# Performance work log

Measured on AMD Instinct MI355X. Metric: run time of the kernel, lower is better.

The kernel has to match this reference:

```python
import jax, jax.numpy as jnp
import numpy as np

L, M, B = 32768, 8, 8192      # lines, max neighbors per line, blocks
LIN, BIN, H = 768, 768, 512   # line_in_dim, block_in_dim, hidden_size
NH, DH = 8, 512 // 8          # heads, head_dim
LN_EPS = 1e-5


def _ln(x, g, b):
    mu = jnp.mean(x, axis=-1, keepdims=True)
    var = jnp.mean(jnp.square(x - mu), axis=-1, keepdims=True)
    return (x - mu) * jax.lax.rsqrt(var + LN_EPS) * g + b


def setup_inputs() -> dict:
    key = jax.random.key(0)
    ks = jax.random.split(key, 12)
    w = lambda k, shape, fan: jax.random.normal(k, shape, jnp.float32) * (fan ** -0.5)
    return {
        'global_lines': jax.random.normal(ks[0], (L, LIN), jnp.float32),
        'block_reprs': jax.random.normal(ks[1], (B, BIN), jnp.float32),
        'Wq': w(ks[2], (H, LIN), LIN),            # q_proj (no bias)
        'Wkv': w(ks[3], (H, BIN), BIN),           # kv_proj (no bias)
        'qn_g': jnp.ones((H,), jnp.float32), 'qn_b': jnp.zeros((H,), jnp.float32),
        'kvn_g': jnp.ones((H,), jnp.float32), 'kvn_b': jnp.zeros((H,), jnp.float32),
        'in_proj_w': w(ks[4], (3 * H, H), H), 'in_proj_b': jnp.zeros((3 * H,), jnp.float32),
        'out_w': w(ks[5], (H, H), H), 'out_b': jnp.zeros((H,), jnp.float32),
        'p1_w': w(ks[6], (H, 2 * H), 2 * H), 'p1_b': jnp.zeros((H,), jnp.float32),
        'ln1_g': jnp.ones((H,), jnp.float32), 'ln1_b': jnp.zeros((H,), jnp.float32),
        'p2_w': w(ks[7], (H, H), H), 'p2_b': jnp.zeros((H,), jnp.float32),
        'ln2_g': jnp.ones((H,), jnp.float32), 'ln2_b': jnp.zeros((H,), jnp.float32),
        'head_w': w(ks[8], (1, H), H), 'head_b': jnp.zeros((1,), jnp.float32),
        'K_indices': jax.random.randint(ks[9], (L, M), 0, B, jnp.int32),
        'neighbor_counts': jnp.clip(jax.random.randint(ks[10], (L,), 0, M + 1, jnp.int32), 1, M),
    }


def reference(global_lines, block_reprs, Wq, Wkv, qn_g, qn_b, kvn_g, kvn_b,
              in_proj_w, in_proj_b, out_w, out_b,
              p1_w, p1_b, ln1_g, ln1_b, p2_w, p2_b, ln2_g, ln2_b,
              head_w, head_b, K_indices, neighbor_counts):
    # q = LN(q_proj(lines))                              [L, H]
    q = _ln(global_lines @ Wq.T, qn_g, qn_b)
    # gather neighbor block reprs, project, LN           [L, M, H]
    kv = _ln(block_reprs[K_indices] @ Wkv.T, kvn_g, kvn_b)
    pad = jnp.arange(M)[None, :] >= neighbor_counts[:, None]  # True = padded key

    # torch nn.MultiheadAttention with query length 1 per line
    wq_i, wk_i, wv_i = jnp.split(in_proj_w, 3, axis=0)
    bq_i, bk_i, bv_i = jnp.split(in_proj_b, 3, axis=0)
    qh = (q @ wq_i.T + bq_i).reshape(L, NH, DH)
    kh = (kv @ wk_i.T + bk_i).reshape(L, M, NH, DH)
    vh = (kv @ wv_i.T + bv_i).reshape(L, M, NH, DH)
    scores = jnp.einsum('lhd,lmhd->lhm', qh, kh) / np.float32(np.sqrt(DH))
    scores = jnp.where(pad[:, None, :], jnp.finfo(scores.dtype).min, scores)
    attn = jax.nn.softmax(scores, axis=-1)
    ctx = jnp.einsum('lhm,lmhd->lhd', attn, vh).reshape(L, H)
    attn_out = ctx @ out_w.T + out_b

    # line_proj: Linear(2H->H) + LN + GELU + residual(Linear + LN + GELU)
    x = jnp.concatenate([q, attn_out], axis=-1)
    x = jax.nn.gelu(_ln(x @ p1_w.T + p1_b, ln1_g, ln1_b), approximate=False)
    x = x + jax.nn.gelu(_ln(x @ p2_w.T + p2_b, ln2_g, ln2_b), approximate=False)
    logits = (x @ head_w.T + head_b)[:, 0]
    return jax.nn.sigmoid(logits)
```

## Files before the change

### kernel.cpp

```cpp
#include <hip/hip_runtime.h>
#include <math.h>


typedef unsigned short u16;
typedef unsigned int u32;
using bf16x8 = __attribute__((ext_vector_type(8))) __bf16;
using u16x8  = __attribute__((ext_vector_type(8))) u16;
using f32x4  = __attribute__((ext_vector_type(4))) float;

__device__ __forceinline__ u16 f2bf(float f) {
    u32 u = __builtin_bit_cast(u32, f);
    u32 r = u + 0x7fffu + ((u >> 16) & 1u);
    return (u16)(r >> 16);
}
__device__ __forceinline__ float bf2f(u16 h) {
    return __builtin_bit_cast(float, (u32)h << 16);
}
__device__ __forceinline__ float gelu_exact(float x) {
    return 0.5f * x * (1.0f + erff(x * 0.70710678118654752440f));
}

__device__ __forceinline__ float breduce1(float s0, float* sm) {
    #pragma unroll
    for (int off = 32; off > 0; off >>= 1) s0 += __shfl_down(s0, off);
    const int lane = threadIdx.x & 63, w = threadIdx.x >> 6;
    __syncthreads();
    if (lane == 0) sm[w] = s0;
    __syncthreads();
    return sm[0] + sm[1] + sm[2] + sm[3];
}

struct CvtJobs {
    const float* s[5];
    u16* d[5];
    int cum[6];
};
__global__ __launch_bounds__(256) void cvt_multi(CvtJobs j)
{
    const int g = blockIdx.x * 256 + threadIdx.x;
    if (g >= j.cum[5]) return;
    int seg = 0;
    #pragma unroll
    for (int k = 1; k < 5; ++k) seg += (g >= j.cum[k]);
    const int q = g - j.cum[seg];
    const float4 v = *reinterpret_cast<const float4*>(j.s[seg] + q * 4);
    ushort4 o = make_ushort4(f2bf(v.x), f2bf(v.y), f2bf(v.z), f2bf(v.w));
    *reinterpret_cast<ushort4*>(j.d[seg] + q * 4) = o;
}

__global__ __launch_bounds__(256) void fold_w2(
    const float* __restrict__ p1w, const float* __restrict__ outw,
    u16* __restrict__ p1cb)
{
    __shared__ float As[16][65];
    __shared__ float Bs[16][65];
    const int tx = threadIdx.x & 15, ty = threadIdx.x >> 4;
    const int i0 = blockIdx.y * 64, j0 = blockIdx.x * 64;
    const int lr = threadIdx.x >> 2;
    const int lc = (threadIdx.x & 3) * 4;
    const int kr = threadIdx.x >> 4;
    const int jc = (threadIdx.x & 15) * 4;
    float acc[4][4] = {};
    for (int k0 = 0; k0 < 512; k0 += 16) {
        const float4 av = *reinterpret_cast<const float4*>(
            p1w + (size_t)(i0 + lr) * 1024 + 512 + k0 + lc);
        As[lc + 0][lr] = av.x; As[lc + 1][lr] = av.y;
        As[lc + 2][lr] = av.z; As[lc + 3][lr] = av.w;
        const float4 bv = *reinterpret_cast<const float4*>(
            outw + (size_t)(k0 + kr) * 512 + j0 + jc);
        Bs[kr][jc + 0] = bv.x; Bs[kr][jc + 1] = bv.y;
        Bs[kr][jc + 2] = bv.z; Bs[kr][jc + 3] = bv.w;
        __syncthreads();
        #pragma unroll
        for (int kk = 0; kk < 16; ++kk) {
            float a[4], b[4];
            #pragma unroll
            for (int i = 0; i < 4; ++i) a[i] = As[kk][ty * 4 + i];
            #pragma unroll
            for (int jj = 0; jj < 4; ++jj) b[jj] = Bs[kk][tx * 4 + jj];
            #pragma unroll
            for (int i = 0; i < 4; ++i)
                #pragma unroll
                for (int jj = 0; jj < 4; ++jj)
                    acc[i][jj] = fmaf(a[i], b[jj], acc[i][jj]);
        }
        __syncthreads();
    }
    #pragma unroll
    for (int i = 0; i < 4; ++i)
        #pragma unroll
        for (int jj = 0; jj < 4; ++jj)
            p1cb[(size_t)(i0 + ty * 4 + i) * 1024 + 512 + j0 + tx * 4 + jj] =
                f2bf(acc[i][jj]);
}

__global__ __launch_bounds__(64) void fold_bias(
    const float* __restrict__ p1w, const float* __restrict__ outb,
    const float* __restrict__ p1b, float* __restrict__ bias2)
{
    const int i = blockIdx.x, lane = threadIdx.x;
    float s = 0.0f;
    #pragma unroll
    for (int k = lane; k < 512; k += 64)
        s += p1w[(size_t)i * 1024 + 512 + k] * outb[k];
    #pragma unroll
    for (int off = 32; off > 0; off >>= 1) s += __shfl_down(s, off);
    if (lane == 0) bias2[i] = s + p1b[i];
}

template<int A_MODE, bool STATS>
__global__ __launch_bounds__(256) void gemm_bf16(
    const void* __restrict__ A1v, const void* __restrict__ A2v, int K1, int K,
    const u16* __restrict__ W, const float* __restrict__ bias,
    u16* __restrict__ C, int N, float* __restrict__ stats)
{
    __shared__ __bf16 As[128 * 32];
    __shared__ __bf16 Ws[128 * 32];
    const int tid = threadIdx.x;
    const int w = tid >> 6, lane = tid & 63;

    const u32 nx = gridDim.x;
    const u32 orig = blockIdx.y * nx + blockIdx.x;
    const u32 nwg = nx * gridDim.y;
    const u32 wgid = (orig & 7u) * (nwg >> 3) + (orig >> 3);
    const int bx = wgid % nx;
    const int row0 = (int)(wgid / nx) * 128;
    const int col0 = bx * 128;

    const int wr = (w >> 1) * 64, wc = (w & 1) * 64;
    const int fr = lane & 15, fg = lane >> 4;

    int srow[2], scol[2], soff[2];
    #pragma unroll
    for (int c = 0; c < 2; ++c) {
        const int bo = w * 2048 + c * 1024 + lane * 16;
        srow[c] = bo >> 6;
        scol[c] = (bo & 63) >> 1;
        soff[c] = (w * 2048 + c * 1024) >> 1;
    }
    const int ar = tid >> 1;
    const int ac = (tid & 1) * 16;

    f32x4 acc[4][4] = {};

    for (int k0 = 0; k0 < K; k0 += 32) {
        if (A_MODE == 1) {
            const float* Af = (const float*)A1v;
            const float* src = Af + (size_t)(row0 + ar) * K + k0 + ac;
            const float4 v0 = *reinterpret_cast<const float4*>(src);
            const float4 v1 = *reinterpret_cast<const float4*>(src + 4);
            const float4 v2 = *reinterpret_cast<const float4*>(src + 8);
            const float4 v3 = *reinterpret_cast<const float4*>(src + 12);
            u16x8 p0, p1;
            p0[0] = f2bf(v0.x); p0[1] = f2bf(v0.y); p0[2] = f2bf(v0.z); p0[3] = f2bf(v0.w);
            p0[4] = f2bf(v1.x); p0[5] = f2bf(v1.y); p0[6] = f2bf(v1.z); p0[7] = f2bf(v1.w);
            p1[0] = f2bf(v2.x); p1[1] = f2bf(v2.y); p1[2] = f2bf(v2.z); p1[3] = f2bf(v2.w);
            p1[4] = f2bf(v3.x); p1[5] = f2bf(v3.y); p1[6] = f2bf(v3.z); p1[7] = f2bf(v3.w);
            *reinterpret_cast<u16x8*>((u16*)As + ar * 32 + ac) = p0;
            *reinterpret_cast<u16x8*>((u16*)As + ar * 32 + ac + 8) = p1;
        } else {
            #pragma unroll
            for (int c = 0; c < 2; ++c) {
                const u16* asrc;
                if (A_MODE == 2) {
                    const bool first = (k0 < K1);
                    const u16* base = first ? (const u16*)A1v : (const u16*)A2v;
                    const int ldk = first ? K1 : (K - K1);
                    const int kk  = first ? k0 : (k0 - K1);
                    asrc = base + (size_t)(row0 + srow[c]) * ldk + kk + scol[c];
                } else {
                    asrc = (const u16*)A1v + (size_t)(row0 + srow[c]) * K + k0 + scol[c];
                }
                __builtin_amdgcn_global_load_lds(
                    (const __attribute__((address_space(1))) u32*)asrc,
                    (__attribute__((address_space(3))) u32*)(As + soff[c]), 16, 0, 0);
            }
        }
        #pragma unroll
        for (int c = 0; c < 2; ++c) {
            const u16* wsrc = W + (size_t)(col0 + srow[c]) * K + k0 + scol[c];
            __builtin_amdgcn_global_load_lds(
                (const __attribute__((address_space(1))) u32*)wsrc,
                (__attribute__((address_space(3))) u32*)(Ws + soff[c]), 16, 0, 0);
        }
        __syncthreads();

        bf16x8 af[4], bfr[4];
        #pragma unroll
        for (int m = 0; m < 4; ++m) {
            af[m]  = *(const bf16x8*)(As + (wr + m * 16 + fr) * 32 + fg * 8);
            bfr[m] = *(const bf16x8*)(Ws + (wc + m * 16 + fr) * 32 + fg * 8);
        }
        #pragma unroll
        for (int m = 0; m < 4; ++m)
            #pragma unroll
            for (int n = 0; n < 4; ++n)
                acc[m][n] = __builtin_amdgcn_mfma_f32_16x16x32_bf16(
                    af[m], bfr[n], acc[m][n], 0, 0, 0);
        __syncthreads();
    }

    if (bias) {
        #pragma unroll
        for (int n = 0; n < 4; ++n) {
            const float bv = bias[col0 + wc + n * 16 + fr];
            #pragma unroll
            for (int m = 0; m < 4; ++m)
                #pragma unroll
                for (int r = 0; r < 4; ++r)
                    acc[m][n][r] += bv;
        }
    }

    #pragma unroll
    for (int m = 0; m < 4; ++m)
        #pragma unroll
        for (int n = 0; n < 4; ++n) {
            const int col = col0 + wc + n * 16 + fr;
            #pragma unroll
            for (int r = 0; r < 4; ++r) {
                const int row = row0 + wr + m * 16 + fg * 4 + r;
                C[(size_t)row * N + col] = f2bf(acc[m][n][r]);
            }
        }

    if (STATS) {
        float ps[4][4], pq[4][4];
        #pragma unroll
        for (int m = 0; m < 4; ++m)
            #pragma unroll
            for (int r = 0; r < 4; ++r) {
                float s = 0.0f, q2 = 0.0f;
                #pragma unroll
                for (int n = 0; n < 4; ++n) {
                    const float v = acc[m][n][r];
                    s += v; q2 = fmaf(v, v, q2);
                }
                ps[m][r] = s; pq[m][r] = q2;
            }
        #pragma unroll
        for (int off = 1; off < 16; off <<= 1)
            #pragma unroll
            for (int m = 0; m < 4; ++m)
                #pragma unroll
                for (int r = 0; r < 4; ++r) {
                    ps[m][r] += __shfl_xor(ps[m][r], off);
                    pq[m][r] += __shfl_xor(pq[m][r], off);
                }
        if (fr == 0) {
            const int cb = bx * 2 + (w & 1);
            #pragma unroll
            for (int m = 0; m < 4; ++m)
                #pragma unroll
                for (int r = 0; r < 4; ++r) {
                    const int row = row0 + wr + m * 16 + fg * 4 + r;
                    *reinterpret_cast<float2*>(stats + ((size_t)row * 8 + cb) * 2) =
                        make_float2(ps[m][r], pq[m][r]);
                }
        }
    }
}

template<bool GELU>
__global__ __launch_bounds__(256) void ln_rows_s(
    u16* __restrict__ X, const float* __restrict__ stats,
    const float* __restrict__ g, const float* __restrict__ b)
{
    const size_t row = blockIdx.x;
    float s = 0.0f, q2 = 0.0f;
    #pragma unroll
    for (int cb = 0; cb < 8; ++cb) {
        s  += stats[(row * 8 + cb) * 2];
        q2 += stats[(row * 8 + cb) * 2 + 1];
    }
    const float mu = s * (1.0f / 512.0f);
    const float var = q2 * (1.0f / 512.0f) - mu * mu;
    const float rs = rsqrtf(var + 1e-5f);
    const int t = threadIdx.x;
    const ushort2 xv = *reinterpret_cast<const ushort2*>(X + row * 512 + 2 * t);
    const float2 gg = *reinterpret_cast<const float2*>(g + 2 * t);
    const float2 bb = *reinterpret_cast<const float2*>(b + 2 * t);
    float y0 = (bf2f(xv.x) - mu) * rs * gg.x + bb.x;
    float y1 = (bf2f(xv.y) - mu) * rs * gg.y + bb.y;
    if (GELU) { y0 = gelu_exact(y0); y1 = gelu_exact(y1); }
    *reinterpret_cast<ushort2*>(X + row * 512 + 2 * t) = make_ushort2(f2bf(y0), f2bf(y1));
}

__global__ __launch_bounds__(512) void attn_kernel(
    const u16* __restrict__ qh, const u16* __restrict__ kvb,
    const int* __restrict__ kidx, const int* __restrict__ ncnt,
    u16* __restrict__ ctx)
{
    const int head = threadIdx.x >> 6;
    const int lane = threadIdx.x & 63;
    const int mi = lane & 7, dg = lane >> 3;
    const bool b0 = (mi & 1), b1 = (mi & 2), b2 = (mi & 4);
    const int doff = (b0 ? 4 : 0) + (b1 ? 2 : 0) + (b2 ? 1 : 0);

    for (int l = blockIdx.x; l < 32768; l += gridDim.x) {
        const int cnt = ncnt[l];
        const int idx = kidx[l * 8 + mi];
        const size_t kvbase = (size_t)idx * 1024 + head * 64 + dg * 8;

        const u16x8 qv = *(const u16x8*)(qh + (size_t)l * 512 + head * 64 + dg * 8);
        const u16x8 kv = *(const u16x8*)(kvb + kvbase);
        const u16x8 vv = *(const u16x8*)(kvb + kvbase + 512);

        float p = 0.0f;
        #pragma unroll
        for (int jj = 0; jj < 8; ++jj) p = fmaf(bf2f(qv[jj]), bf2f(kv[jj]), p);
        p += __shfl_xor(p, 8); p += __shfl_xor(p, 16); p += __shfl_xor(p, 32);

        float s = (mi < cnt) ? p * 0.125f : -3.402823466e38f;
        float mx = s;
        mx = fmaxf(mx, __shfl_xor(mx, 1));
        mx = fmaxf(mx, __shfl_xor(mx, 2));
        mx = fmaxf(mx, __shfl_xor(mx, 4));
        const float e = __expf(s - mx);
        float den = e;
        den += __shfl_xor(den, 1); den += __shfl_xor(den, 2); den += __shfl_xor(den, 4);
        const float wgt = e / den;

        float c[8];
        #pragma unroll
        for (int jj = 0; jj < 8; ++jj) c[jj] = wgt * bf2f(vv[jj]);

        #pragma unroll
        for (int jj = 0; jj < 4; ++jj) {
            const float snd = b0 ? c[jj] : c[jj + 4];
            const float rec = __shfl_xor(snd, 1);
            c[jj] = (b0 ? c[jj + 4] : c[jj]) + rec;
        }
        #pragma unroll
        for (int jj = 0; jj < 2; ++jj) {
            const float snd = b1 ? c[jj] : c[jj + 2];
            const float rec = __shfl_xor(snd, 2);
            c[jj] = (b1 ? c[jj + 2] : c[jj]) + rec;
        }
        {
            const float snd = b2 ? c[0] : c[1];
            const float rec = __shfl_xor(snd, 4);
            c[0] = (b2 ? c[1] : c[0]) + rec;
        }
        ctx[(size_t)l * 512 + head * 64 + dg * 8 + doff] = f2bf(c[0]);
    }
}

__global__ __launch_bounds__(256) void final_head_s(
    const u16* __restrict__ h1, const u16* __restrict__ h2raw,
    const float* __restrict__ stats,
    const float* __restrict__ g, const float* __restrict__ b,
    const float* __restrict__ hw, const float* __restrict__ hb,
    float* __restrict__ out)
{
    __shared__ float sm[4];
    const size_t row = blockIdx.x;
    float s = 0.0f, q2 = 0.0f;
    #pragma unroll
    for (int cb = 0; cb < 8; ++cb) {
        s  += stats[(row * 8 + cb) * 2];
        q2 += stats[(row * 8 + cb) * 2 + 1];
    }
    const float mu = s * (1.0f / 512.0f);
    const float var = q2 * (1.0f / 512.0f) - mu * mu;
    const float rs = rsqrtf(var + 1e-5f);
    const int t = threadIdx.x;
    const ushort2 xv = *reinterpret_cast<const ushort2*>(h2raw + row * 512 + 2 * t);
    const ushort2 hv = *reinterpret_cast<const ushort2*>(h1 + row * 512 + 2 * t);
    const float2 gg = *reinterpret_cast<const float2*>(g + 2 * t);
    const float2 bb = *reinterpret_cast<const float2*>(b + 2 * t);
    const float2 hwv = *reinterpret_cast<const float2*>(hw + 2 * t);
    const float y0 = bf2f(hv.x) + gelu_exact((bf2f(xv.x) - mu) * rs * gg.x + bb.x);
    const float y1 = bf2f(hv.y) + gelu_exact((bf2f(xv.y) - mu) * rs * gg.y + bb.y);
    const float d = breduce1(y0 * hwv.x + y1 * hwv.y, sm);
    if (t == 0) out[row] = 1.0f / (1.0f + expf(-(d + hb[0])));
}

extern "C" void kernel_launch(void* const* d_in, const int* in_sizes, int n_in,
                              void* d_out, int out_size, void* d_ws, size_t ws_size,
                              hipStream_t stream)
{
    const float* lines  = (const float*)d_in[0];
    const float* blocks = (const float*)d_in[1];
    const float* Wq     = (const float*)d_in[2];
    const float* Wkv    = (const float*)d_in[3];
    const float* qn_g   = (const float*)d_in[4];
    const float* qn_b   = (const float*)d_in[5];
    const float* kvn_g  = (const float*)d_in[6];
    const float* kvn_b  = (const float*)d_in[7];
    const float* in_w   = (const float*)d_in[8];
    const float* in_b   = (const float*)d_in[9];
    const float* out_w  = (const float*)d_in[10];
    const float* out_b  = (const float*)d_in[11];
    const float* p1_w   = (const float*)d_in[12];
    const float* p1_b   = (const float*)d_in[13];
    const float* ln1_g  = (const float*)d_in[14];
    const float* ln1_b  = (const float*)d_in[15];
    const float* p2_w   = (const float*)d_in[16];
    const float* p2_b   = (const float*)d_in[17];
    const float* ln2_g  = (const float*)d_in[18];
    const float* ln2_b  = (const float*)d_in[19];
    const float* head_w = (const float*)d_in[20];
    const float* head_b = (const float*)d_in[21];
    const int*   kidx   = (const int*)d_in[22];
    const int*   ncnt   = (const int*)d_in[23];
    float* out = (float*)d_out;

    char* wsb = (char*)d_ws;
    u16* qb    = (u16*)(wsb);
    u16* qhb   = (u16*)(wsb + (32ull << 20));
    u16* ctxb  = (u16*)(wsb + (64ull << 20));
    u16* kvbb  = (u16*)(wsb + (96ull << 20));
    u16* bkvb  = (u16*)(wsb + (112ull << 20));
    float* stats_q   = (float*)(wsb + (120ull << 20));
    float* stats_h1  = (float*)(wsb + (124ull << 20));
    float* stats_h2  = (float*)(wsb + (128ull << 20));
    float* stats_bkv = (float*)(wsb + (132ull << 20));
    u16* Wqb   = (u16*)(wsb + (136ull << 20));
    u16* Wkvb  = Wqb + 512 * 768;
    u16* inwb  = Wkvb + 512 * 768;
    u16* p1cb  = inwb + 1536 * 512;
    u16* p2wb  = p1cb + 512 * 1024;
    float* bias2f = (float*)(p2wb + 512 * 512);

    {
        CvtJobs j;
        const float* ss[5] = { Wq, Wkv, in_w, p1_w, p2_w };
        u16* dd[5] = { Wqb, Wkvb, inwb, p1cb, p2wb };
        const int nn[5] = { 512 * 768, 512 * 768, 1536 * 512, 512 * 1024, 512 * 512 };
        int c = 0;
        for (int k = 0; k < 5; ++k) { j.s[k] = ss[k]; j.d[k] = dd[k]; j.cum[k] = c; c += nn[k] / 4; }
        j.cum[5] = c;
        cvt_multi<<<(c + 255) / 256, 256, 0, stream>>>(j);
    }
    fold_w2<<<dim3(8, 8), 256, 0, stream>>>(p1_w, out_w, p1cb);
    fold_bias<<<512, 64, 0, stream>>>(p1_w, out_b, p1_b, bias2f);

    gemm_bf16<1, true><<<dim3(4, 64), 256, 0, stream>>>(
        blocks, nullptr, 768, 768, Wkvb, nullptr, bkvb, 512, stats_bkv);
    ln_rows_s<false><<<8192, 256, 0, stream>>>(bkvb, stats_bkv, kvn_g, kvn_b);
    gemm_bf16<0, false><<<dim3(8, 64), 256, 0, stream>>>(
        bkvb, nullptr, 512, 512, inwb + 512 * 512, in_b + 512, kvbb, 1024, nullptr);
    gemm_bf16<1, true><<<dim3(4, 256), 256, 0, stream>>>(
        lines, nullptr, 768, 768, Wqb, nullptr, qb, 512, stats_q);
    ln_rows_s<false><<<32768, 256, 0, stream>>>(qb, stats_q, qn_g, qn_b);
    gemm_bf16<0, false><<<dim3(4, 256), 256, 0, stream>>>(
        qb, nullptr, 512, 512, inwb, in_b, qhb, 512, nullptr);
    attn_kernel<<<2048, 512, 0, stream>>>(qhb, kvbb, kidx, ncnt, ctxb);
    gemm_bf16<2, true><<<dim3(4, 256), 256, 0, stream>>>(
        qb, ctxb, 512, 1024, p1cb, bias2f, qhb, 512, stats_h1);
    ln_rows_s<true><<<32768, 256, 0, stream>>>(qhb, stats_h1, ln1_g, ln1_b);
    gemm_bf16<0, true><<<dim3(4, 256), 256, 0, stream>>>(
        qhb, nullptr, 512, 512, p2wb, p2_b, ctxb, 512, stats_h2);
    final_head_s<<<32768, 256, 0, stream>>>(qhb, ctxb, stats_h2, ln2_g, ln2_b,
                                            head_w, head_b, out);
}
```

Before: 467.2 us.

## Double-buffer LDS tiles in bf16 GEMM to overlap loads with MFMA

Doubles the shared-memory A and W tiles and prefetches the next K-slice into the alternate buffer while MFMAs run on the current one. For fp32 A inputs, the global loads are issued early and the bf16 conversion and LDS store are deferred until after the MFMAs. This removes one barrier per iteration and hides global-load latency. It costs twice the LDS per block, which may reduce occupancy, and more registers for the prefetched fp32 values.

Result: faster. 449.5 us (-3.8%).

```diff
diff --git a/kernel.cpp b/kernel.cpp
--- a/kernel.cpp
+++ b/kernel.cpp
@@ -114,8 +114,8 @@
     const u16* __restrict__ W, const float* __restrict__ bias,
     u16* __restrict__ C, int N, float* __restrict__ stats)
 {
-    __shared__ __bf16 As[128 * 32];
-    __shared__ __bf16 Ws[128 * 32];
+    __shared__ __bf16 As[2 * 128 * 32];
+    __shared__ __bf16 Ws[2 * 128 * 32];
     const int tid = threadIdx.x;
     const int w = tid >> 6, lane = tid & 63;
 
@@ -142,22 +142,15 @@
     const int ac = (tid & 1) * 16;
 
     f32x4 acc[4][4] = {};
-
-    for (int k0 = 0; k0 < K; k0 += 32) {
+    float4 av0, av1, av2, av3;
+
+    auto stage_issue = [&](int k0, int buf) {
         if (A_MODE == 1) {
-            const float* Af = (const float*)A1v;
-            const float* src = Af + (size_t)(row0 + ar) * K + k0 + ac;
-            const float4 v0 = *reinterpret_cast<const float4*>(src);
-            const float4 v1 = *reinterpret_cast<const float4*>(src + 4);
-            const float4 v2 = *reinterpret_cast<const float4*>(src + 8);
-            const float4 v3 = *reinterpret_cast<const float4*>(src + 12);
-            u16x8 p0, p1;
-            p0[0] = f2bf(v0.x); p0[1] = f2bf(v0.y); p0[2] = f2bf(v0.z); p0[3] = f2bf(v0.w);
-            p0[4] = f2bf(v1.x); p0[5] = f2bf(v1.y); p0[6] = f2bf(v1.z); p0[7] = f2bf(v1.w);
-            p1[0] = f2bf(v2.x); p1[1] = f2bf(v2.y); p1[2] = f2bf(v2.z); p1[3] = f2bf(v2.w);
-            p1[4] = f2bf(v3.x); p1[5] = f2bf(v3.y); p1[6] = f2bf(v3.z); p1[7] = f2bf(v3.w);
-            *reinterpret_cast<u16x8*>((u16*)As + ar * 32 + ac) = p0;
-            *reinterpret_cast<u16x8*>((u16*)As + ar * 32 + ac + 8) = p1;
+            const float* src = (const float*)A1v + (size_t)(row0 + ar) * K + k0 + ac;
+            av0 = *reinterpret_cast<const float4*>(src);
+            av1 = *reinterpret_cast<const float4*>(src + 4);
+            av2 = *reinterpret_cast<const float4*>(src + 8);
+            av3 = *reinterpret_cast<const float4*>(src + 12);
         } else {
             #pragma unroll
             for (int c = 0; c < 2; ++c) {
@@ -173,7 +166,8 @@
                 }
                 __builtin_amdgcn_global_load_lds(
                     (const __attribute__((address_space(1))) u32*)asrc,
-                    (__attribute__((address_space(3))) u32*)(As + soff[c]), 16, 0, 0);
+                    (__attribute__((address_space(3))) u32*)(As + buf * 4096 + soff[c]),
+                    16, 0, 0);
             }
         }
         #pragma unroll
@@ -181,15 +175,36 @@
             const u16* wsrc = W + (size_t)(col0 + srow[c]) * K + k0 + scol[c];
             __builtin_amdgcn_global_load_lds(
                 (const __attribute__((address_space(1))) u32*)wsrc,
-                (__attribute__((address_space(3))) u32*)(Ws + soff[c]), 16, 0, 0);
-        }
-        __syncthreads();
+                (__attribute__((address_space(3))) u32*)(Ws + buf * 4096 + soff[c]),
+                16, 0, 0);
+        }
+    };
+    auto stage_write_a = [&](int buf) {
+        u16x8 p0, p1;
+        p0[0] = f2bf(av0.x); p0[1] = f2bf(av0.y); p0[2] = f2bf(av0.z); p0[3] = f2bf(av0.w);
+        p0[4] = f2bf(av1.x); p0[5] = f2bf(av1.y); p0[6] = f2bf(av1.z); p0[7] = f2bf(av1.w);
+        p1[0] = f2bf(av2.x); p1[1] = f2bf(av2.y); p1[2] = f2bf(av2.z); p1[3] = f2bf(av2.w);
+        p1[4] = f2bf(av3.x); p1[5] = f2bf(av3.y); p1[6] = f2bf(av3.z); p1[7] = f2bf(av3.w);
+        *reinterpret_cast<u16x8*>((u16*)As + buf * 4096 + ar * 32 + ac) = p0;
+        *reinterpret_cast<u16x8*>((u16*)As + buf * 4096 + ar * 32 + ac + 8) = p1;
+    };
+
+    const int NT = K >> 5;
+    int cur = 0;
+
+    stage_issue(0, 0);
+    if (A_MODE == 1) stage_write_a(0);
+    __syncthreads();
+
+    for (int t = 0; t < NT; ++t) {
+        const bool have_next = (t + 1 < NT);
+        if (have_next) stage_issue((t + 1) << 5, cur ^ 1);
 
         bf16x8 af[4], bfr[4];
         #pragma unroll
         for (int m = 0; m < 4; ++m) {
-            af[m]  = *(const bf16x8*)(As + (wr + m * 16 + fr) * 32 + fg * 8);
-            bfr[m] = *(const bf16x8*)(Ws + (wc + m * 16 + fr) * 32 + fg * 8);
+            af[m]  = *(const bf16x8*)(As + cur * 4096 + (wr + m * 16 + fr) * 32 + fg * 8);
+            bfr[m] = *(const bf16x8*)(Ws + cur * 4096 + (wc + m * 16 + fr) * 32 + fg * 8);
         }
         #pragma unroll
         for (int m = 0; m < 4; ++m)
@@ -197,7 +212,10 @@
             for (int n = 0; n < 4; ++n)
                 acc[m][n] = __builtin_amdgcn_mfma_f32_16x16x32_bf16(
                     af[m], bfr[n], acc[m][n], 0, 0, 0);
+
+        if (have_next && A_MODE == 1) stage_write_a(cur ^ 1);
         __syncthreads();
+        cur ^= 1;
     }
 
     if (bias) {
```
